# Optimization experiments

Hardware: AMD Instinct MI355X
Metric: run time of the kernel (lower is better)

## Reference

```python
import jax, jax.numpy as jnp
import numpy as np

SEQ_LEN = 180
LATENT = 128
HIDDEN = 256
BATCH = 8192


def setup_inputs() -> dict:
    key = jax.random.key(0)
    ks = jax.random.split(key, 9)
    s = 1.0 / np.sqrt(HIDDEN)
    return {
        "z": jax.random.normal(ks[0], (BATCH, LATENT), jnp.float32),
        "fc_w": jax.random.normal(ks[1], (HIDDEN, LATENT), jnp.float32) * (1.0 / np.sqrt(LATENT)),
        "fc_b": jax.random.normal(ks[2], (HIDDEN,), jnp.float32) * 0.1,
        "w_ih": jax.random.normal(ks[3], (3 * HIDDEN, 2), jnp.float32) * s,
        "b_ih": jax.random.normal(ks[4], (3 * HIDDEN,), jnp.float32) * s,
        "w_hh": jax.random.normal(ks[5], (3 * HIDDEN, HIDDEN), jnp.float32) * s,
        "b_hh": jax.random.normal(ks[6], (3 * HIDDEN,), jnp.float32) * s,
        "out_w": jax.random.normal(ks[7], (2, HIDDEN), jnp.float32) * s,
        "out_b": jax.random.normal(ks[8], (2,), jnp.float32) * 0.1,
    }


def reference(z, fc_w, fc_b, w_ih, b_ih, w_hh, b_hh, out_w, out_b):
    # h0 = tanh(fc(z))  -> [B, H]
    h0 = jnp.tanh(z @ fc_w.T + fc_b)
    B = z.shape[0]
    # GRU input is all-zeros, so input-hidden gates are a constant bias: [B, 3H]
    gi = jnp.zeros((B, 2), z.dtype) @ w_ih.T + b_ih
    gi_r, gi_z, gi_n = jnp.split(gi, 3, axis=-1)

    def step(h, _):
        gh = h @ w_hh.T + b_hh                 # [B, 3H]
        gh_r, gh_z, gh_n = jnp.split(gh, 3, axis=-1)
        r = jax.nn.sigmoid(gi_r + gh_r)
        zg = jax.nn.sigmoid(gi_z + gh_z)
        n = jnp.tanh(gi_n + r * gh_n)
        h_new = (1.0 - zg) * n + zg * h
        return h_new, h_new

    _, hs = jax.lax.scan(step, h0, None, length=SEQ_LEN)  # [T, B, H]
    hs = jnp.swapaxes(hs, 0, 1)                            # [B, T, H]
    return hs @ out_w.T + out_b                            # [B, T, 2]
```

## Files before the change

kernel.cpp:

```cpp
#include <hip/hip_runtime.h>
#include <hip/hip_bf16.h>

#define T_SEQ  180
#define LATENT 128
#define HIDDEN 256

typedef __attribute__((ext_vector_type(8))) short  short8;
typedef __attribute__((ext_vector_type(4))) float  floatx4;
typedef __attribute__((ext_vector_type(4))) int    intx4;

#define LOG2E 1.4426950408889634f

#define WQ_OFF    0
#define FCW_OFF   196608
#define SCW_OFF   262144
#define OUTW_OFF  265216
#define SWOUT_OFF 269312

#define H8_STRIDE  272
#define H8B_OFF    8704
#define OBUF_OFF   17408
#define SMEM_BYTES 19456

__device__ __forceinline__ unsigned short f2bf(float f) {
    unsigned int u = __float_as_uint(f);
    u += 0x7fffu + ((u >> 16) & 1u);
    return (unsigned short)(u >> 16);
}

__global__ void pack_scales(const float* __restrict__ whh, float* __restrict__ scales) {
    int wid  = blockIdx.x * 4 + (threadIdx.x >> 6);
    int lane = threadIdx.x & 63;
    const float* src = whh + (size_t)wid * 256 + lane * 4;
    float m = 0.0f;
#pragma unroll
    for (int j = 0; j < 4; ++j) m = fmaxf(m, fabsf(src[j]));
#pragma unroll
    for (int d = 1; d < 64; d <<= 1) m = fmaxf(m, __shfl_xor(m, d, 64));
    if (lane == 0) scales[wid] = m;
}

__global__ void pack_whh_i8(const float* __restrict__ whh, const float* __restrict__ scales,
                            signed char* __restrict__ dst) {
    int tid  = blockIdx.x * blockDim.x + threadIdx.x;
    int lane = tid & 63;
    int frag = tid >> 6;
    int kc   = frag & 3;
    int sub  = (frag >> 2) % 6;
    int w    = frag / 24;
    int g = sub >> 1, cs = sub & 1;
    int col  = w * 32 + cs * 16 + (lane & 15);
    int jout = g * 256 + col;
    int k0   = kc * 64 + ((lane >> 4) << 4);
    const float* src = whh + (size_t)jout * 256 + k0;
    float inv = 127.0f / scales[jout];
    signed char q[16];
#pragma unroll
    for (int j = 0; j < 16; ++j) {
        float v = __builtin_rintf(src[j] * inv);
        v = fminf(fmaxf(v, -127.0f), 127.0f);
        q[j] = (signed char)(int)v;
    }
    *(intx4*)(dst + (size_t)frag * 1024 + lane * 16) = *(intx4*)q;
}

__global__ void pack_fcw(const float* __restrict__ fcw, unsigned short* __restrict__ dst) {
    int tid  = blockIdx.x * blockDim.x + threadIdx.x;
    int lane = tid & 63;
    int frag = tid >> 6;
    int kc   = frag & 3;
    int cs   = (frag >> 2) & 1;
    int w    = frag >> 3;
    int col  = w * 32 + cs * 16 + (lane & 15);
    int k0   = kc * 32 + ((lane >> 4) << 3);
    const float* src = fcw + col * 128 + k0;
    unsigned int u[4];
#pragma unroll
    for (int j = 0; j < 4; ++j)
        u[j] = (unsigned int)f2bf(src[2 * j]) | ((unsigned int)f2bf(src[2 * j + 1]) << 16);
    *(uint4*)(dst + frag * 512 + lane * 8) = make_uint4(u[0], u[1], u[2], u[3]);
}

__global__ void pack_outw_i8(const float* __restrict__ out_w,
                             signed char* __restrict__ dst, float* __restrict__ swout) {
    __shared__ float sw[2];
    int tid = threadIdx.x;
    if (tid < 128) {
        int o = tid >> 6, lane = tid & 63;
        const float* src = out_w + o * 256 + lane * 4;
        float m = 0.0f;
#pragma unroll
        for (int j = 0; j < 4; ++j) m = fmaxf(m, fabsf(src[j]));
#pragma unroll
        for (int d = 1; d < 64; d <<= 1) m = fmaxf(m, __shfl_xor(m, d, 64));
        if (lane == 0) { sw[o] = m; swout[o] = m; }
    }
    __syncthreads();
    int sl = tid >> 6, lane = tid & 63;
    int n  = lane & 15;
    int k0 = sl * 64 + ((lane >> 4) << 4);
    signed char q[16];
#pragma unroll
    for (int j = 0; j < 16; ++j) {
        float v = 0.0f;
        if (n < 2) {
            v = __builtin_rintf(out_w[n * 256 + k0 + j] * (127.0f / sw[n]));
            v = fminf(fmaxf(v, -127.0f), 127.0f);
        }
        q[j] = (signed char)(int)v;
    }
    *(intx4*)(dst + sl * 1024 + lane * 16) = *(intx4*)q;
}

__global__ __launch_bounds__(1024, 4) void gru_main(
    const float* __restrict__ z,
    const float* __restrict__ fc_b,
    const float* __restrict__ b_ih,
    const float* __restrict__ b_hh,
    const float* __restrict__ out_b,
    const unsigned char* __restrict__ ws,
    float* __restrict__ out)
{
    extern __shared__ unsigned char smem[];
    signed char* h8a   = (signed char*)smem;
    signed char* h8b   = (signed char*)(smem + H8B_OFF);
    int*         obufI = (int*)(smem + OBUF_OFF);

    const int tid  = threadIdx.x;
    const int lane = tid & 63;
    const int wv   = tid >> 6;
    const int cg   = wv;
    const int l15  = lane & 15;
    const int qd   = lane >> 4;
    const int rh   = (wv >> 2) & 1;
    const int sl   = wv & 3;
    const int rb   = blockIdx.x * 32;

    intx4 wq[12];
#pragma unroll
    for (int g = 0; g < 3; ++g)
#pragma unroll
        for (int kc = 0; kc < 4; ++kc)
            wq[g * 4 + kc] = *(const intx4*)(ws + WQ_OFF
                + (size_t)((((cg >> 1) * 6 + g * 2 + (cg & 1)) * 4 + kc)) * 1024 + lane * 16);

    intx4 bproj = *(const intx4*)(ws + OUTW_OFF + sl * 1024 + lane * 16);
    const float* swout = (const float*)(ws + SWOUT_OFF);
    float pscF = swout[tid & 1] * (1.0f / 16129.0f);

    const float* scales = (const float*)(ws + SCW_OFF);
    float ncbrE, ncbzE, bhnE2, binE2, fcbE2, nscqrE, nscqzE, scqnE2;
    {
        int col = cg * 16 + l15;
        ncbrE  = -(b_ih[col]       + b_hh[col])       * LOG2E;
        ncbzE  = -(b_ih[256 + col] + b_hh[256 + col]) * LOG2E;
        binE2  = b_ih[512 + col] * (2.0f * LOG2E);
        bhnE2  = b_hh[512 + col] * (2.0f * LOG2E);
        fcbE2  = fc_b[col] * (2.0f * LOG2E);
        nscqrE = -scales[col]       * (LOG2E / 16129.0f);
        nscqzE = -scales[256 + col] * (LOG2E / 16129.0f);
        scqnE2 = scales[512 + col] * (2.0f * LOG2E / 16129.0f);
    }
    float ob = out_b[tid & 1];

    const int rlW = ((tid - 512) >> 1) & 31;
    const int o8  = tid & 1;
    float* opW8 = out + (size_t)(rb + rlW) * (T_SEQ * 2) + o8;

    floatx4 a0f[2];
#pragma unroll
    for (int rt = 0; rt < 2; ++rt) a0f[rt] = (floatx4){0.f, 0.f, 0.f, 0.f};
#pragma unroll
    for (int kc = 0; kc < 4; ++kc) {
        short8 bfr = *(const short8*)(ws + FCW_OFF + (size_t)(cg * 4 + kc) * 1024 + lane * 16);
#pragma unroll
        for (int rt = 0; rt < 2; ++rt) {
            const float* zp = z + (size_t)(rb + rt * 16 + l15) * LATENT + kc * 32 + qd * 8;
            short8 afr;
#pragma unroll
            for (int j = 0; j < 8; ++j) afr[j] = (short)f2bf(zp[j]);
            a0f[rt] = __builtin_amdgcn_mfma_f32_16x16x32_bf16(afr, bfr, a0f[rt], 0, 0, 0);
        }
    }

    float hm[2][4];
#pragma unroll
    for (int rt = 0; rt < 2; ++rt)
#pragma unroll
        for (int r = 0; r < 4; ++r) {
            float u = __builtin_amdgcn_rcpf(1.0f + __builtin_amdgcn_exp2f(
                          __builtin_fmaf(a0f[rt][r], 2.0f * LOG2E, fcbE2)));
            float h = __builtin_fmaf(-254.0f, u, 127.0f);
            hm[rt][r] = h;
            h8a[(rt * 16 + qd * 4 + r) * H8_STRIDE + cg * 16 + l15] =
                (signed char)(int)__builtin_rintf(h);
        }
    __syncthreads();

#define GRU_STEP(H8P, H8N, PP, DO_STASH, DO_FLUSH)                                   \
    {                                                                                \
        intx4 acc[6];                                                                \
        _Pragma("unroll")                                                            \
        for (int s_ = 0; s_ < 6; ++s_) acc[s_] = (intx4){0, 0, 0, 0};                \
        _Pragma("unroll")                                                            \
        for (int kc = 0; kc < 4; ++kc) {                                             \
            intx4 a80 = *(const intx4*)&(H8P)[(0  + l15) * H8_STRIDE + kc * 64 + qd * 16]; \
            intx4 a81 = *(const intx4*)&(H8P)[(16 + l15) * H8_STRIDE + kc * 64 + qd * 16]; \
            _Pragma("unroll")                                                        \
            for (int g = 0; g < 3; ++g) {                                            \
                acc[g]     = __builtin_amdgcn_mfma_i32_16x16x64_i8(a80, wq[g * 4 + kc], acc[g],     0, 0, 0); \
                acc[3 + g] = __builtin_amdgcn_mfma_i32_16x16x64_i8(a81, wq[g * 4 + kc], acc[3 + g], 0, 0, 0); \
            }                                                                        \
        }                                                                            \
        intx4 pj = (intx4){0, 0, 0, 0};                                              \
        if (DO_STASH && wv < 8) {                                                    \
            intx4 a8p = *(const intx4*)&(H8P)[(rh * 16 + l15) * H8_STRIDE + sl * 64 + qd * 16]; \
            pj = __builtin_amdgcn_mfma_i32_16x16x64_i8(a8p, bproj, pj, 0, 0, 0);     \
        }                                                                            \
        if (DO_FLUSH && tid >= 512 && tid < 576) {                                   \
            int base = (((PP) ^ 1) * 2 + (rlW >> 4)) * 128 + (rlW & 15) * 2 + o8;    \
            int s_ = obufI[base] + obufI[base + 32] + obufI[base + 64] + obufI[base + 96]; \
            *opW8 = __builtin_fmaf((float)s_, pscF, ob);                             \
            opW8 += 2;                                                               \
        }                                                                            \
        _Pragma("unroll")                                                            \
        for (int rt = 0; rt < 2; ++rt)                                               \
            _Pragma("unroll")                                                        \
            for (int r = 0; r < 4; ++r) {                                            \
                float Ar  = __builtin_amdgcn_exp2f(                                  \
                                __builtin_fmaf((float)acc[rt * 3 + 0][r], nscqrE, ncbrE)); \
                float Az  = __builtin_amdgcn_exp2f(                                  \
                                __builtin_fmaf((float)acc[rt * 3 + 1][r], nscqzE, ncbzE)); \
                float xn2 = __builtin_fmaf((float)acc[rt * 3 + 2][r], scqnE2, bhnE2);\
                float dr = 1.0f + Ar, dz = 1.0f + Az;                                \
                float q_  = __builtin_amdgcn_rcpf(dr * dz);          \
                float gr = q_ * dz, gz = q_ * dr;                                    \
                float u_ = __builtin_amdgcn_rcpf(1.0f + __builtin_amdgcn_exp2f(      \
                               __builtin_fmaf(gr, xn2, binE2)));                     \
                float gn = __builtin_fmaf(-254.0f, u_, 127.0f);        \
                float h  = __builtin_fmaf(gz, hm[rt][r] - gn, gn);                   \
                hm[rt][r] = h;                                                       \
                (H8N)[(rt * 16 + qd * 4 + r) * H8_STRIDE + cg * 16 + l15] =          \
                    (signed char)(int)__builtin_rintf(h);                            \
            }                                                                        \
        if (DO_STASH && wv < 8 && l15 < 2) {                                         \
            _Pragma("unroll")                                                        \
            for (int r = 0; r < 4; ++r)                                              \
                obufI[((PP) * 2 + rh) * 128 + sl * 32 + (qd * 4 + r) * 2 + l15] = pj[r]; \
        }                                                                            \
        __syncthreads();                                                             \
    }

    GRU_STEP(h8a, h8b, 0, 0, 0)
    GRU_STEP(h8b, h8a, 1, 1, 0)
#pragma unroll 1
    for (int t2 = 0; t2 < 89; ++t2) {
        GRU_STEP(h8a, h8b, 0, 1, 1)
        GRU_STEP(h8b, h8a, 1, 1, 1)
    }
#undef GRU_STEP

    if (tid < 64) {
        int rl = tid >> 1, o = tid & 1;
        int base = (1 * 2 + (rl >> 4)) * 128 + (rl & 15) * 2 + o;
        int s = obufI[base] + obufI[base + 32] + obufI[base + 64] + obufI[base + 96];
        out[(size_t)(rb + rl) * (T_SEQ * 2) + 178 * 2 + o] =
            __builtin_fmaf((float)s, pscF, ob);
    }
    if (wv < 8) {
        intx4 a8p = *(const intx4*)&h8a[(rh * 16 + l15) * H8_STRIDE + sl * 64 + qd * 16];
        intx4 pj = (intx4){0, 0, 0, 0};
        pj = __builtin_amdgcn_mfma_i32_16x16x64_i8(a8p, bproj, pj, 0, 0, 0);
        if (l15 < 2)
#pragma unroll
            for (int r = 0; r < 4; ++r)
                obufI[(0 * 2 + rh) * 128 + sl * 32 + (qd * 4 + r) * 2 + l15] = pj[r];
    }
    __syncthreads();
    if (tid < 64) {
        int rl = tid >> 1, o = tid & 1;
        int base = (0 * 2 + (rl >> 4)) * 128 + (rl & 15) * 2 + o;
        int s = obufI[base] + obufI[base + 32] + obufI[base + 64] + obufI[base + 96];
        out[(size_t)(rb + rl) * (T_SEQ * 2) + 179 * 2 + o] =
            __builtin_fmaf((float)s, pscF, ob);
    }
}

extern "C" void kernel_launch(void* const* d_in, const int* in_sizes, int n_in,
                              void* d_out, int out_size, void* d_ws, size_t ws_size,
                              hipStream_t stream) {
    const float* z     = (const float*)d_in[0];
    const float* fc_w  = (const float*)d_in[1];
    const float* fc_b  = (const float*)d_in[2];
    const float* b_ih  = (const float*)d_in[4];
    const float* w_hh  = (const float*)d_in[5];
    const float* b_hh  = (const float*)d_in[6];
    const float* out_w = (const float*)d_in[7];
    const float* out_b = (const float*)d_in[8];
    float* out = (float*)d_out;
    unsigned char* ws = (unsigned char*)d_ws;

    hipFuncSetAttribute((const void*)gru_main,
                        hipFuncAttributeMaxDynamicSharedMemorySize, SMEM_BYTES);

    pack_scales<<<192, 256, 0, stream>>>(w_hh, (float*)(ws + SCW_OFF));
    pack_whh_i8<<<48, 256, 0, stream>>>(w_hh, (const float*)(ws + SCW_OFF),
                                        (signed char*)(ws + WQ_OFF));
    pack_fcw<<<16, 256, 0, stream>>>(fc_w, (unsigned short*)(ws + FCW_OFF));
    pack_outw_i8<<<1, 256, 0, stream>>>(out_w, (signed char*)(ws + OUTW_OFF),
                                        (float*)(ws + SWOUT_OFF));
    gru_main<<<256, 1024, SMEM_BYTES, stream>>>(z, fc_b, b_ih, b_hh, out_b, ws, out);
}
```

Before: 472.0 us.

## Software-pipeline GRU step across two row halves to overlap MFMA with gate math

Each GRU timestep is split into two half-steps, one per 16-row tile, so the int8 MFMAs for one tile are interleaved with the sigmoid/tanh gate updates of the other tile. This is meant to hide transcendental and VALU latency behind matrix-core work. The cost is twice as many block barriers per step. The output-stash buffer shrinks to a single slot, which reduces shared memory. Float-to-int8 rounding also switches from rintf plus a convert to a magic-number add-and-bitcast.

```diff
diff --git a/kernel.cpp b/kernel.cpp
--- a/kernel.cpp
+++ b/kernel.cpp
@@ -20,7 +20,7 @@
 #define H8_STRIDE  272
 #define H8B_OFF    8704
 #define OBUF_OFF   17408
-#define SMEM_BYTES 19456
+#define SMEM_BYTES 18432
 
 __device__ __forceinline__ unsigned short f2bf(float f) {
     unsigned int u = __float_as_uint(f);
@@ -163,8 +163,13 @@
     }
     float ob = out_b[tid & 1];
 
+    const int rdOff = l15 * H8_STRIDE + qd * 16;
+    const int pjOff = (rh * 16 + l15) * H8_STRIDE + sl * 64 + qd * 16;
+    const int wrOff = (qd * 4) * H8_STRIDE + cg * 16 + l15;
+
     const int rlW = ((tid - 512) >> 1) & 31;
     const int o8  = tid & 1;
+    const int fbase = (rlW >> 4) * 128 + (rlW & 15) * 2 + o8;
     float* opW8 = out + (size_t)(rb + rlW) * (T_SEQ * 2) + o8;
 
     floatx4 a0f[2];
@@ -193,97 +198,123 @@
             float h = __builtin_fmaf(-254.0f, u, 127.0f);
             hm[rt][r] = h;
             h8a[(rt * 16 + qd * 4 + r) * H8_STRIDE + cg * 16 + l15] =
-                (signed char)(int)__builtin_rintf(h);
+                (signed char)__float_as_uint(h + 12582912.0f);
         }
     __syncthreads();
 
-#define GRU_STEP(H8P, H8N, PP, DO_STASH, DO_FLUSH)                                   \
-    {                                                                                \
-        intx4 acc[6];                                                                \
-        _Pragma("unroll")                                                            \
-        for (int s_ = 0; s_ < 6; ++s_) acc[s_] = (intx4){0, 0, 0, 0};                \
-        _Pragma("unroll")                                                            \
-        for (int kc = 0; kc < 4; ++kc) {                                             \
-            intx4 a80 = *(const intx4*)&(H8P)[(0  + l15) * H8_STRIDE + kc * 64 + qd * 16]; \
-            intx4 a81 = *(const intx4*)&(H8P)[(16 + l15) * H8_STRIDE + kc * 64 + qd * 16]; \
-            _Pragma("unroll")                                                        \
-            for (int g = 0; g < 3; ++g) {                                            \
-                acc[g]     = __builtin_amdgcn_mfma_i32_16x16x64_i8(a80, wq[g * 4 + kc], acc[g],     0, 0, 0); \
-                acc[3 + g] = __builtin_amdgcn_mfma_i32_16x16x64_i8(a81, wq[g * 4 + kc], acc[3 + g], 0, 0, 0); \
-            }                                                                        \
-        }                                                                            \
-        intx4 pj = (intx4){0, 0, 0, 0};                                              \
-        if (DO_STASH && wv < 8) {                                                    \
-            intx4 a8p = *(const intx4*)&(H8P)[(rh * 16 + l15) * H8_STRIDE + sl * 64 + qd * 16]; \
-            pj = __builtin_amdgcn_mfma_i32_16x16x64_i8(a8p, bproj, pj, 0, 0, 0);     \
-        }                                                                            \
-        if (DO_FLUSH && tid >= 512 && tid < 576) {                                   \
-            int base = (((PP) ^ 1) * 2 + (rlW >> 4)) * 128 + (rlW & 15) * 2 + o8;    \
-            int s_ = obufI[base] + obufI[base + 32] + obufI[base + 64] + obufI[base + 96]; \
-            *opW8 = __builtin_fmaf((float)s_, pscF, ob);                             \
-            opW8 += 2;                                                               \
-        }                                                                            \
-        _Pragma("unroll")                                                            \
-        for (int rt = 0; rt < 2; ++rt)                                               \
-            _Pragma("unroll")                                                        \
-            for (int r = 0; r < 4; ++r) {                                            \
-                float Ar  = __builtin_amdgcn_exp2f(                                  \
-                                __builtin_fmaf((float)acc[rt * 3 + 0][r], nscqrE, ncbrE)); \
-                float Az  = __builtin_amdgcn_exp2f(                                  \
-                                __builtin_fmaf((float)acc[rt * 3 + 1][r], nscqzE, ncbzE)); \
-                float xn2 = __builtin_fmaf((float)acc[rt * 3 + 2][r], scqnE2, bhnE2);\
-                float dr = 1.0f + Ar, dz = 1.0f + Az;                                \
-                float q_  = __builtin_amdgcn_rcpf(dr * dz);          \
-                float gr = q_ * dz, gz = q_ * dr;                                    \
-                float u_ = __builtin_amdgcn_rcpf(1.0f + __builtin_amdgcn_exp2f(      \
-                               __builtin_fmaf(gr, xn2, binE2)));                     \
-                float gn = __builtin_fmaf(-254.0f, u_, 127.0f);        \
-                float h  = __builtin_fmaf(gz, hm[rt][r] - gn, gn);                   \
-                hm[rt][r] = h;                                                       \
-                (H8N)[(rt * 16 + qd * 4 + r) * H8_STRIDE + cg * 16 + l15] =          \
-                    (signed char)(int)__builtin_rintf(h);                            \
-            }                                                                        \
-        if (DO_STASH && wv < 8 && l15 < 2) {                                         \
-            _Pragma("unroll")                                                        \
-            for (int r = 0; r < 4; ++r)                                              \
-                obufI[((PP) * 2 + rh) * 128 + sl * 32 + (qd * 4 + r) * 2 + l15] = pj[r]; \
-        }                                                                            \
-        __syncthreads();                                                             \
-    }
-
-    GRU_STEP(h8a, h8b, 0, 0, 0)
-    GRU_STEP(h8b, h8a, 1, 1, 0)
+    intx4 acc0[3], acc1[3];
+
+#define HUPD(ACC, RT, R, DSTP)                                                   \
+    {                                                                            \
+        float Ar  = __builtin_amdgcn_exp2f(                                      \
+                        __builtin_fmaf((float)(ACC)[0][R], nscqrE, ncbrE));      \
+        float Az  = __builtin_amdgcn_exp2f(                                      \
+                        __builtin_fmaf((float)(ACC)[1][R], nscqzE, ncbzE));      \
+        float xn2 = __builtin_fmaf((float)(ACC)[2][R], scqnE2, bhnE2);           \
+        float dr = 1.0f + Ar, dz = 1.0f + Az;                                    \
+        float q_ = __builtin_amdgcn_rcpf(dr * dz);                               \
+        float gr = q_ * dz, gz = q_ * dr;                                        \
+        float u_ = __builtin_amdgcn_rcpf(1.0f + __builtin_amdgcn_exp2f(          \
+                       __builtin_fmaf(gr, xn2, binE2)));                         \
+        float gn = __builtin_fmaf(-254.0f, u_, 127.0f);                          \
+        float h  = __builtin_fmaf(gz, hm[RT][R] - gn, gn);                       \
+        hm[RT][R] = h;                                                           \
+        *(DSTP) = (signed char)__float_as_uint(h + 12582912.0f);                 \
+    }
+
+#define REGION_A(BUF, DO_V1, DO_FLUSH)                                           \
+    {                                                                            \
+        _Pragma("unroll")                                                        \
+        for (int g = 0; g < 3; ++g) acc0[g] = (intx4){0, 0, 0, 0};               \
+        const signed char* rp = (BUF) + rdOff;                                   \
+        signed char*       wp = (BUF) + wrOff + 16 * H8_STRIDE;                  \
+        _Pragma("unroll")                                                        \
+        for (int kc = 0; kc < 4; ++kc) {                                         \
+            intx4 a8 = *(const intx4*)(rp + kc * 64);                            \
+            acc0[0] = __builtin_amdgcn_mfma_i32_16x16x64_i8(a8, wq[kc],     acc0[0], 0, 0, 0); \
+            acc0[1] = __builtin_amdgcn_mfma_i32_16x16x64_i8(a8, wq[4 + kc], acc0[1], 0, 0, 0); \
+            acc0[2] = __builtin_amdgcn_mfma_i32_16x16x64_i8(a8, wq[8 + kc], acc0[2], 0, 0, 0); \
+            if (DO_V1) { HUPD(acc1, 1, kc, wp + kc * H8_STRIDE) }                \
+        }                                                                        \
+        if (DO_FLUSH && tid >= 512 && tid < 576) {                               \
+            int s_ = obufI[fbase] + obufI[fbase + 32]                            \
+                   + obufI[fbase + 64] + obufI[fbase + 96];                      \
+            *opW8 = __builtin_fmaf((float)s_, pscF, ob);                         \
+            opW8 += 2;                                                           \
+        }                                                                        \
+        __syncthreads();                                                         \
+    }
+
+#define REGION_C(BUFR, BUFW, DO_PJ)                                              \
+    {                                                                            \
+        _Pragma("unroll")                                                        \
+        for (int g = 0; g < 3; ++g) acc1[g] = (intx4){0, 0, 0, 0};               \
+        const signed char* rp = (BUFR) + rdOff + 16 * H8_STRIDE;                 \
+        signed char*       wp = (BUFW) + wrOff;                                  \
+        intx4 pj = (intx4){0, 0, 0, 0};                                          \
+        if (DO_PJ && wv < 8) {                                                   \
+            intx4 a8p = *(const intx4*)((BUFR) + pjOff);                         \
+            pj = __builtin_amdgcn_mfma_i32_16x16x64_i8(a8p, bproj, pj, 0, 0, 0); \
+        }                                                                        \
+        _Pragma("unroll")                                                        \
+        for (int kc = 0; kc < 4; ++kc) {                                         \
+            intx4 a8 = *(const intx4*)(rp + kc * 64);                            \
+            acc1[0] = __builtin_amdgcn_mfma_i32_16x16x64_i8(a8, wq[kc],     acc1[0], 0, 0, 0); \
+            acc1[1] = __builtin_amdgcn_mfma_i32_16x16x64_i8(a8, wq[4 + kc], acc1[1], 0, 0, 0); \
+            acc1[2] = __builtin_amdgcn_mfma_i32_16x16x64_i8(a8, wq[8 + kc], acc1[2], 0, 0, 0); \
+            HUPD(acc0, 0, kc, wp + kc * H8_STRIDE)                               \
+        }                                                                        \
+        if (DO_PJ && wv < 8 && l15 < 2) {                                        \
+            _Pragma("unroll")                                                    \
+            for (int r = 0; r < 4; ++r)                                          \
+                obufI[(rh * 4 + sl) * 32 + (qd * 4 + r) * 2 + l15] = pj[r];      \
+        }                                                                        \
+        __syncthreads();                                                         \
+    }
+
+    REGION_A(h8a, 0, 0)
+    REGION_C(h8a, h8b, 0)
+    REGION_A(h8b, 1, 0)
+    REGION_C(h8b, h8a, 1)
+
 #pragma unroll 1
     for (int t2 = 0; t2 < 89; ++t2) {
-        GRU_STEP(h8a, h8b, 0, 1, 1)
-        GRU_STEP(h8b, h8a, 1, 1, 1)
-    }
-#undef GRU_STEP
-
-    if (tid < 64) {
-        int rl = tid >> 1, o = tid & 1;
-        int base = (1 * 2 + (rl >> 4)) * 128 + (rl & 15) * 2 + o;
-        int s = obufI[base] + obufI[base + 32] + obufI[base + 64] + obufI[base + 96];
-        out[(size_t)(rb + rl) * (T_SEQ * 2) + 178 * 2 + o] =
-            __builtin_fmaf((float)s, pscF, ob);
+        REGION_A(h8a, 1, 1)
+        REGION_C(h8a, h8b, 1)
+        REGION_A(h8b, 1, 1)
+        REGION_C(h8b, h8a, 1)
+    }
+
+    {
+        signed char* wp = h8a + wrOff + 16 * H8_STRIDE;
+#pragma unroll
+        for (int r = 0; r < 4; ++r) { HUPD(acc1, 1, r, wp + r * H8_STRIDE) }
+        if (tid >= 512 && tid < 576) {
+            int s_ = obufI[fbase] + obufI[fbase + 32]
+                   + obufI[fbase + 64] + obufI[fbase + 96];
+            *opW8 = __builtin_fmaf((float)s_, pscF, ob);
+            opW8 += 2;
+        }
+        __syncthreads();
     }
     if (wv < 8) {
-        intx4 a8p = *(const intx4*)&h8a[(rh * 16 + l15) * H8_STRIDE + sl * 64 + qd * 16];
+        intx4 a8p = *(const intx4*)(h8a + pjOff);
         intx4 pj = (intx4){0, 0, 0, 0};
         pj = __builtin_amdgcn_mfma_i32_16x16x64_i8(a8p, bproj, pj, 0, 0, 0);
         if (l15 < 2)
 #pragma unroll
             for (int r = 0; r < 4; ++r)
-                obufI[(0 * 2 + rh) * 128 + sl * 32 + (qd * 4 + r) * 2 + l15] = pj[r];
+                obufI[(rh * 4 + sl) * 32 + (qd * 4 + r) * 2 + l15] = pj[r];
     }
     __syncthreads();
-    if (tid < 64) {
-        int rl = tid >> 1, o = tid & 1;
-        int base = (0 * 2 + (rl >> 4)) * 128 + (rl & 15) * 2 + o;
-        int s = obufI[base] + obufI[base + 32] + obufI[base + 64] + obufI[base + 96];
-        out[(size_t)(rb + rl) * (T_SEQ * 2) + 179 * 2 + o] =
-            __builtin_fmaf((float)s, pscF, ob);
-    }
+    if (tid >= 512 && tid < 576) {
+        int s_ = obufI[fbase] + obufI[fbase + 32]
+               + obufI[fbase + 64] + obufI[fbase + 96];
+        *opW8 = __builtin_fmaf((float)s_, pscF, ob);
+    }
+#undef REGION_C
+#undef REGION_A
+#undef HUPD
 }
 
 extern "C" void kernel_launch(void* const* d_in, const int* in_sizes, int n_in,
```

Result: no change. 464.6 us (-1.6%).
